# Performance work log

Hardware: AMD Instinct MI355X
Metric: run time of the kernel (lower is better)

The kernel has to match this reference:

```python
import jax, jax.numpy as jnp
import numpy as np

EPS = 1e-9  # Dice BatchNormalization epsilon


def dice(x, alpha):
    # Keras BatchNormalization(axis=-1, center=False, scale=False) in training
    # mode: normalize over all axes except the last using batch statistics.
    mean = jnp.mean(x, axis=(0, 1), keepdims=True)
    var = jnp.var(x, axis=(0, 1), keepdims=True)
    x_normed = (x - mean) * jax.lax.rsqrt(var + EPS)
    p = jax.nn.sigmoid(x_normed)
    return alpha * (1.0 - p) * x + p * x


def setup_inputs() -> dict:
    key = jax.random.key(0)
    ks = jax.random.split(key, 11)
    B, T, D = 512, 2048, 20
    keys_ = jax.random.normal(ks[0], (B, T, D), dtype=jnp.float32)
    query = jax.random.normal(ks[1], (B, 1, D), dtype=jnp.float32)
    mask = jax.random.randint(ks[2], (B, T), 0, 2) > 0
    # DNN tower weights: hidden dims 80 -> 32 -> 16, attention head 16 -> 1
    W0 = jax.random.normal(ks[3], (80, 32), dtype=jnp.float32) * 0.1
    b0 = jax.random.normal(ks[4], (32,), dtype=jnp.float32) * 0.1
    a0 = jax.random.normal(ks[5], (32,), dtype=jnp.float32) * 0.1
    W1 = jax.random.normal(ks[6], (32, 16), dtype=jnp.float32) * 0.1
    b1 = jax.random.normal(ks[7], (16,), dtype=jnp.float32) * 0.1
    a1 = jax.random.normal(ks[8], (16,), dtype=jnp.float32) * 0.1
    wk = jax.random.normal(ks[9], (16, 1), dtype=jnp.float32) * 0.1
    bk = jax.random.normal(ks[10], (1,), dtype=jnp.float32) * 0.1
    return {"keys": keys_, "query": query, "mask": mask,
            "W0": W0, "b0": b0, "a0": a0,
            "W1": W1, "b1": b1, "a1": a1,
            "wk": wk, "bk": bk}


def reference(keys, query, mask, W0, b0, a0, W1, b1, a1, wk, bk):
    B, T, D = keys.shape
    # repeat query along the key/time axis: [B,1,D] -> [B,T,D]
    queries = jnp.broadcast_to(query, (B, T, D))
    # local-activation features: [B,T,4D] = [B,T,80]
    att = jnp.concatenate([queries, keys, queries - keys, queries * keys], axis=-1)
    # DNN tower with Dice activations (dropout is identity at inference)
    h = dice(att @ W0 + b0, a0)   # [B,T,32]
    h = dice(h @ W1 + b1, a1)     # [B,T,16]
    score = h @ wk + bk           # [B,T,1]
    outputs = jnp.transpose(score, (0, 2, 1))  # [B,1,T]
    # NOTE: the original code computes the masked scores into self.outputs but
    # then (weight_normalization=False, return_score=False) overwrites it with
    # matmul(outputs, keys) using the UNMASKED scores -- we reproduce that.
    return jnp.matmul(outputs, keys)  # [B,1,D]
```

## Files before the change

kernel.cpp:

```cpp
#include <hip/hip_runtime.h>


#define BB 512
#define TT 2048
#define DD 20
#define C0 32
#define C1 16

#define NTH 256
#define NPOS 4
#define POSB (NTH * NPOS)
#define NBLK (TT / POSB)

#define WS_SUM0 0
#define WS_SQ0 32
#define WS_SUM1 64
#define WS_SQ1 80
#define WS_SCALE0 96
#define WS_SHIFT0 128
#define WS_SCALE1 160
#define WS_SHIFT1 176
#define WS_BLOB 192
#define BLOB_J 24
#define BLOB_B (C0 * BLOB_J)

#define PIN(x) asm volatile("" : "+v"(x))

__device__ __forceinline__ float fast_sigmoid(float x) {
    return __builtin_amdgcn_rcpf(1.0f + __expf(-x));
}

__device__ __forceinline__ void load_krow(const float* __restrict__ row,
                                          float* kk) {
    const float4* kr = (const float4*)row;
    float4 a = kr[0], b = kr[1], c = kr[2], d = kr[3], e = kr[4];
    kk[0] = a.x; kk[1] = a.y; kk[2] = a.z; kk[3] = a.w;
    kk[4] = b.x; kk[5] = b.y; kk[6] = b.z; kk[7] = b.w;
    kk[8] = c.x; kk[9] = c.y; kk[10] = c.z; kk[11] = c.w;
    kk[12] = d.x; kk[13] = d.y; kk[14] = d.z; kk[15] = d.w;
    kk[16] = e.x; kk[17] = e.y; kk[18] = e.z; kk[19] = e.w;
}

__global__ void prep_kernel(const float* __restrict__ query,
                            const float* __restrict__ W0,
                            const float* __restrict__ b0,
                            float* __restrict__ blob) {
    const int b = blockIdx.x * 2 + (threadIdx.x >> 5);
    const int j = threadIdx.x & 31;
    float cj = b0[j];
    float* dst = blob + (size_t)b * BLOB_B + j * BLOB_J;
#pragma unroll
    for (int d = 0; d < DD; ++d) {
        float w_q = W0[d * C0 + j];
        float w_k = W0[(DD + d) * C0 + j];
        float w_d = W0[(2 * DD + d) * C0 + j];
        float w_p = W0[(3 * DD + d) * C0 + j];
        float qd = query[b * DD + d];
        dst[d] = w_k - w_d + qd * w_p;
        cj = fmaf(qd, w_q + w_d, cj);
    }
    dst[20] = cj;
}

__global__ __launch_bounds__(256, 2) void pass1_kernel(
    const float* __restrict__ keys, const float* __restrict__ blob,
    float* __restrict__ ws) {
    const int b = blockIdx.x >> 2, chunk = blockIdx.x & 3;
    const int tid = threadIdx.x, wave = tid >> 6, lane = tid & 63;
    const int j0 = wave * 8;
    const float* wb = blob + (size_t)b * BLOB_B;
    const float* kbase = keys + ((size_t)b * TT + chunk * (TT / 4)) * DD;

    float wM[8][DD], cj8[8];
#pragma unroll
    for (int jj = 0; jj < 8; ++jj) {
        load_krow(wb + (j0 + jj) * BLOB_J, wM[jj]);
        cj8[jj] = wb[(j0 + jj) * BLOB_J + 20];
    }
#pragma unroll
    for (int jj = 0; jj < 8; ++jj) {
        PIN(cj8[jj]);
#pragma unroll
        for (int d = 0; d < DD; ++d) PIN(wM[jj][d]);
    }

    float s[8], q[8];
#pragma unroll
    for (int v = 0; v < 8; ++v) { s[v] = 0.f; q[v] = 0.f; }

#pragma unroll 1
    for (int it = 0; it < (TT / 4) / 64; ++it) {
        float kk[DD];
        load_krow(kbase + (size_t)(it * 64 + lane) * DD, kk);
#pragma unroll
        for (int jj = 0; jj < 8; ++jj) {
            float h = cj8[jj];
#pragma unroll
            for (int d = 0; d < DD; ++d) h = fmaf(kk[d], wM[jj][d], h);
            s[jj] += h;
            q[jj] = fmaf(h, h, q[jj]);
        }
    }
    float mine = 0.f;
#pragma unroll
    for (int v = 0; v < 16; ++v) {
        float val = (v < 8) ? s[v] : q[v - 8];
#pragma unroll
        for (int o = 32; o >= 1; o >>= 1) val += __shfl_xor(val, o);
        if (lane == v) mine = val;
    }
    __shared__ float red[64];
    if (lane < 16) {
        int j = j0 + (lane & 7);
        red[(lane < 8 ? 0 : 32) + j] = mine;
    }
    __syncthreads();
    if (tid < 64) atomicAdd(&ws[WS_SUM0 + tid], red[tid]);
}

__global__ void finalize_kernel(float* __restrict__ ws, int nch, int sumOff,
                                int sqOff, int scOff, int shOff) {
    int j = threadIdx.x;
    if (j < nch) {
        const float invN = 1.0f / (float)(BB * TT);
        float mean = ws[sumOff + j] * invN;
        float ex2 = ws[sqOff + j] * invN;
        float var = ex2 - mean * mean;
        float sc = rsqrtf(var + 1e-9f);
        ws[scOff + j] = sc;
        ws[shOff + j] = -mean * sc;
    }
}

#define STAGE_WEIGHTS()                                                      \
    for (int idx = tid; idx < C0 * 24; idx += NTH) {                         \
        int j = idx / 24, r = idx - j * 24;                                  \
        float v;                                                             \
        if (r < 21) v = blob[(size_t)b * BLOB_B + j * BLOB_J + r];           \
        else if (r == 21) v = ws[WS_SCALE0 + j];                             \
        else if (r == 22) v = ws[WS_SHIFT0 + j];                             \
        else v = a0[j];                                                      \
        lw[idx] = v;                                                         \
    }                                                                        \
    for (int idx = tid; idx < C0 * C1; idx += NTH) lw1[idx] = W1[idx];

#define LOAD_AND_PIN_KEYS()                                                  \
    const float* kbase = keys + ((size_t)b * TT + chunk * POSB) * DD;        \
    float kk[NPOS][DD];                                                      \
    _Pragma("unroll") for (int pp = 0; pp < NPOS; ++pp)                      \
        load_krow(kbase + (size_t)(tid + pp * NTH) * DD, kk[pp]);            \
    _Pragma("unroll") for (int pp = 0; pp < NPOS; ++pp)                      \
        _Pragma("unroll") for (int d = 0; d < DD; ++d) PIN(kk[pp][d]);

#define TOWER_JLOOP()                                                        \
    _Pragma("unroll 1") for (int j = 0; j < C0; ++j) {                       \
        const float4* wv = (const float4*)&lw[j * 24];                       \
        float4 A = wv[0], B = wv[1], Cc = wv[2], E = wv[3], F = wv[4],       \
               P = wv[5];                                                    \
        const float4* uv = (const float4*)&lw1[j * C1];                      \
        float4 U0 = uv[0], U1 = uv[1], U2 = uv[2], U3 = uv[3];               \
        float wr[DD] = {A.x,  A.y,  A.z,  A.w,  B.x,  B.y,  B.z,             \
                        B.w,  Cc.x, Cc.y, Cc.z, Cc.w, E.x,  E.y,             \
                        E.z,  E.w,  F.x,  F.y,  F.z,  F.w};                  \
        float ur[C1] = {U0.x, U0.y, U0.z, U0.w, U1.x, U1.y, U1.z, U1.w,      \
                        U2.x, U2.y, U2.z, U2.w, U3.x, U3.y, U3.z, U3.w};     \
        float h[NPOS];                                                       \
        _Pragma("unroll") for (int pp = 0; pp < NPOS; ++pp) {                \
            float hh = P.x;                                                  \
            _Pragma("unroll") for (int d = 0; d < DD; ++d)                   \
                hh = fmaf(kk[pp][d], wr[d], hh);                             \
            h[pp] = hh;                                                      \
        }                                                                    \
        _Pragma("unroll") for (int pp = 0; pp < NPOS; ++pp) {                \
            float pr = fast_sigmoid(fmaf(h[pp], P.y, P.z));                  \
            float h0d = h[pp] * (P.w + pr * (1.0f - P.w));                   \
            _Pragma("unroll") for (int c = 0; c < C1; ++c)                   \
                h1[pp][c] = fmaf(h0d, ur[c], h1[pp][c]);                     \
        }                                                                    \
    }

__global__ __launch_bounds__(NTH, 2) void pass2_kernel(
    const float* __restrict__ keys, const float* __restrict__ blob,
    const float* __restrict__ a0, const float* __restrict__ W1,
    const float* __restrict__ b1, float* __restrict__ ws) {
    const int b = blockIdx.x >> 1, chunk = blockIdx.x & 1;
    const int tid = threadIdx.x, wave = tid >> 6, lane = tid & 63;
    __shared__ float lw[C0 * 24];
    __shared__ float lw1[C0 * C1];
    __shared__ float red[4][32];
    STAGE_WEIGHTS()
    __syncthreads();

    LOAD_AND_PIN_KEYS()

    float h1[NPOS][C1];
#pragma unroll
    for (int pp = 0; pp < NPOS; ++pp)
#pragma unroll
        for (int c = 0; c < C1; ++c) h1[pp][c] = 0.f;

    TOWER_JLOOP()

    float s1[C1], q1[C1];
#pragma unroll
    for (int c = 0; c < C1; ++c) {
        float bc = b1[c], sv = 0.f, qv = 0.f;
#pragma unroll
        for (int pp = 0; pp < NPOS; ++pp) {
            float v = h1[pp][c] + bc;
            sv += v;
            qv = fmaf(v, v, qv);
        }
        s1[c] = sv;
        q1[c] = qv;
    }
    float mine = 0.f;
#pragma unroll
    for (int v = 0; v < 32; ++v) {
        float val = (v < C1) ? s1[v] : q1[v - C1];
#pragma unroll
        for (int o = 32; o >= 1; o >>= 1) val += __shfl_xor(val, o);
        if (lane == v) mine = val;
    }
    if (lane < 32) red[wave][lane] = mine;
    __syncthreads();
    if (tid < 32)
        atomicAdd(&ws[WS_SUM1 + tid],
                  red[0][tid] + red[1][tid] + red[2][tid] + red[3][tid]);
}

__global__ __launch_bounds__(NTH, 2) void pass3_kernel(
    const float* __restrict__ keys, const float* __restrict__ blob,
    const float* __restrict__ a0, const float* __restrict__ W1,
    const float* __restrict__ b1, const float* __restrict__ a1,
    const float* __restrict__ wk, const float* __restrict__ bk,
    const float* __restrict__ ws, float* __restrict__ out) {
    const int b = blockIdx.x >> 1, chunk = blockIdx.x & 1;
    const int tid = threadIdx.x, wave = tid >> 6, lane = tid & 63;
    __shared__ float lw[C0 * 24];
    __shared__ float lw1[C0 * C1];
    __shared__ float ld1[C1 * 4];
    __shared__ float red[4][DD];
    STAGE_WEIGHTS()
    if (tid < C1) {
        ld1[tid * 4 + 0] = ws[WS_SCALE1 + tid];
        ld1[tid * 4 + 1] = ws[WS_SHIFT1 + tid];
        ld1[tid * 4 + 2] = a1[tid];
        ld1[tid * 4 + 3] = wk[tid];
    }
    __syncthreads();

    LOAD_AND_PIN_KEYS()

    float h1[NPOS][C1];
#pragma unroll
    for (int pp = 0; pp < NPOS; ++pp)
#pragma unroll
        for (int c = 0; c < C1; ++c) h1[pp][c] = 0.f;

    TOWER_JLOOP()

    const float bkv = bk[0];
    float oacc[DD];
#pragma unroll
    for (int d = 0; d < DD; ++d) oacc[d] = 0.f;
#pragma unroll
    for (int pp = 0; pp < NPOS; ++pp) {
        float score = bkv;
#pragma unroll
        for (int c = 0; c < C1; ++c) {
            float v = h1[pp][c] + b1[c];
            float pr = fast_sigmoid(fmaf(v, ld1[c * 4 + 0], ld1[c * 4 + 1]));
            float al = ld1[c * 4 + 2];
            float hd = v * (al + pr * (1.0f - al));
            score = fmaf(hd, ld1[c * 4 + 3], score);
        }
#pragma unroll
        for (int d = 0; d < DD; ++d) oacc[d] = fmaf(score, kk[pp][d], oacc[d]);
    }
    float mine = 0.f;
#pragma unroll
    for (int v = 0; v < DD; ++v) {
        float val = oacc[v];
#pragma unroll
        for (int o = 32; o >= 1; o >>= 1) val += __shfl_xor(val, o);
        if (lane == v) mine = val;
    }
    if (lane < DD) red[wave][lane] = mine;
    __syncthreads();
    if (tid < DD)
        atomicAdd(&out[b * DD + tid],
                  red[0][tid] + red[1][tid] + red[2][tid] + red[3][tid]);
}

extern "C" void kernel_launch(void* const* d_in, const int* in_sizes, int n_in,
                              void* d_out, int out_size, void* d_ws,
                              size_t ws_size, hipStream_t stream) {
    const float* keys = (const float*)d_in[0];
    const float* query = (const float*)d_in[1];
    const float* W0 = (const float*)d_in[3];
    const float* b0 = (const float*)d_in[4];
    const float* a0 = (const float*)d_in[5];
    const float* W1 = (const float*)d_in[6];
    const float* b1 = (const float*)d_in[7];
    const float* a1 = (const float*)d_in[8];
    const float* wk = (const float*)d_in[9];
    const float* bk = (const float*)d_in[10];
    float* out = (float*)d_out;
    float* ws = (float*)d_ws;
    float* blob = ws + WS_BLOB;

    hipMemsetAsync(ws, 0, 96 * sizeof(float), stream);
    hipMemsetAsync(out, 0, (size_t)out_size * sizeof(float), stream);

    prep_kernel<<<BB / 2, 64, 0, stream>>>(query, W0, b0, blob);

    pass1_kernel<<<BB * 4, 256, 0, stream>>>(keys, blob, ws);
    finalize_kernel<<<1, 32, 0, stream>>>(ws, 32, WS_SUM0, WS_SQ0, WS_SCALE0,
                                          WS_SHIFT0);
    pass2_kernel<<<BB * NBLK, NTH, 0, stream>>>(keys, blob, a0, W1, b1, ws);
    finalize_kernel<<<1, 16, 0, stream>>>(ws, 16, WS_SUM1, WS_SQ1, WS_SCALE1,
                                          WS_SHIFT1);
    pass3_kernel<<<BB * NBLK, NTH, 0, stream>>>(keys, blob, a0, W1, b1, a1, wk,
                                                bk, ws, out);
}
```

Measured before the change: 290.6 us.

## Restructure pass1 per batch, read weights from scalar memory, spread stat atomics

Pass1 now gives one block per batch row. Each thread holds four key rows in registers and loops over all 32 channels, reading the per-batch weights directly from global memory (wave-uniform, so they can go through scalar loads) instead of pinning 160 weights in VGPRs. Passes 2 and 3 drop the shared-memory weight staging and the __syncthreads, and read blob, W1 and stats directly as uniform loads. The statistic atomics are spread over 8 slots to reduce contention, and finalize sums the slots. Pass1 now has fewer blocks (512), which may lower occupancy, and its accumulator register pressure rises.

```diff
diff --git a/kernel.cpp b/kernel.cpp
--- a/kernel.cpp
+++ b/kernel.cpp
@@ -10,17 +10,16 @@
 #define NTH 256
 #define NPOS 4
 #define POSB (NTH * NPOS)
-#define NBLK (TT / POSB)
-
-#define WS_SUM0 0
-#define WS_SQ0 32
-#define WS_SUM1 64
-#define WS_SQ1 80
-#define WS_SCALE0 96
-#define WS_SHIFT0 128
-#define WS_SCALE1 160
-#define WS_SHIFT1 176
-#define WS_BLOB 192
+#define NSLOT 8
+
+#define WS_P1 0
+#define WS_P2 512
+#define WS_SCALE0 768
+#define WS_SHIFT0 800
+#define WS_SCALE1 832
+#define WS_SHIFT1 848
+#define WS_ZERO_N 768
+#define WS_BLOB 896
 #define BLOB_J 24
 #define BLOB_B (C0 * BLOB_J)
 
@@ -62,87 +61,77 @@
     dst[20] = cj;
 }
 
-__global__ __launch_bounds__(256, 2) void pass1_kernel(
+__global__ __launch_bounds__(NTH, 2) void pass1_kernel(
     const float* __restrict__ keys, const float* __restrict__ blob,
-    float* __restrict__ ws) {
-    const int b = blockIdx.x >> 2, chunk = blockIdx.x & 3;
-    const int tid = threadIdx.x, wave = tid >> 6, lane = tid & 63;
-    const int j0 = wave * 8;
-    const float* wb = blob + (size_t)b * BLOB_B;
-    const float* kbase = keys + ((size_t)b * TT + chunk * (TT / 4)) * DD;
-
-    float wM[8][DD], cj8[8];
-#pragma unroll
-    for (int jj = 0; jj < 8; ++jj) {
-        load_krow(wb + (j0 + jj) * BLOB_J, wM[jj]);
-        cj8[jj] = wb[(j0 + jj) * BLOB_J + 20];
-    }
-#pragma unroll
-    for (int jj = 0; jj < 8; ++jj) {
-        PIN(cj8[jj]);
-#pragma unroll
-        for (int d = 0; d < DD; ++d) PIN(wM[jj][d]);
-    }
-
-    float s[8], q[8];
-#pragma unroll
-    for (int v = 0; v < 8; ++v) { s[v] = 0.f; q[v] = 0.f; }
+    float* __restrict__ sums) {
+    const int b = blockIdx.x;
+    const int tid = threadIdx.x, lane = tid & 63;
+    const float* bA = blob + (size_t)b * BLOB_B;
+    const float* kbase = keys + (size_t)b * TT * DD;
+
+    float s[C0], q[C0];
+#pragma unroll
+    for (int j = 0; j < C0; ++j) { s[j] = 0.f; q[j] = 0.f; }
 
 #pragma unroll 1
-    for (int it = 0; it < (TT / 4) / 64; ++it) {
-        float kk[DD];
-        load_krow(kbase + (size_t)(it * 64 + lane) * DD, kk);
-#pragma unroll
-        for (int jj = 0; jj < 8; ++jj) {
-            float h = cj8[jj];
-#pragma unroll
-            for (int d = 0; d < DD; ++d) h = fmaf(kk[d], wM[jj][d], h);
-            s[jj] += h;
-            q[jj] = fmaf(h, h, q[jj]);
-        }
-    }
-    float mine = 0.f;
-#pragma unroll
-    for (int v = 0; v < 16; ++v) {
-        float val = (v < 8) ? s[v] : q[v - 8];
+    for (int r = 0; r < TT / POSB; ++r) {
+        float kk[NPOS][DD];
+#pragma unroll
+        for (int pp = 0; pp < NPOS; ++pp)
+            load_krow(kbase + (size_t)(r * POSB + tid + pp * NTH) * DD,
+                      kk[pp]);
+#pragma unroll
+        for (int pp = 0; pp < NPOS; ++pp)
+#pragma unroll
+            for (int d = 0; d < DD; ++d) PIN(kk[pp][d]);
+#pragma unroll
+        for (int j = 0; j < C0; ++j) {
+            const float* wr = bA + j * BLOB_J;
+            const float cj = wr[20];
+            float sv = 0.f, qv = 0.f;
+#pragma unroll
+            for (int pp = 0; pp < NPOS; ++pp) {
+                float hh = cj;
+#pragma unroll
+                for (int d = 0; d < DD; ++d)
+                    hh = fmaf(kk[pp][d], wr[d], hh);
+                sv += hh;
+                qv = fmaf(hh, hh, qv);
+            }
+            s[j] += sv;
+            q[j] += qv;
+        }
+    }
+    float redv = 0.f;
+#pragma unroll
+    for (int v = 0; v < 2 * C0; ++v) {
+        float val = (v < C0) ? s[v] : q[v - C0];
 #pragma unroll
         for (int o = 32; o >= 1; o >>= 1) val += __shfl_xor(val, o);
-        if (lane == v) mine = val;
-    }
-    __shared__ float red[64];
-    if (lane < 16) {
-        int j = j0 + (lane & 7);
-        red[(lane < 8 ? 0 : 32) + j] = mine;
-    }
-    __syncthreads();
-    if (tid < 64) atomicAdd(&ws[WS_SUM0 + tid], red[tid]);
-}
-
-__global__ void finalize_kernel(float* __restrict__ ws, int nch, int sumOff,
-                                int sqOff, int scOff, int shOff) {
+        if (lane == v) redv = val;
+    }
+    atomicAdd(&sums[WS_P1 + (blockIdx.x & (NSLOT - 1)) * (2 * C0) + lane],
+              redv);
+}
+
+__global__ void finalize_kernel(float* __restrict__ ws, int nch, int srcOff,
+                                int scOff, int shOff) {
     int j = threadIdx.x;
     if (j < nch) {
+        float s = 0.f, q = 0.f;
+#pragma unroll
+        for (int k = 0; k < NSLOT; ++k) {
+            s += ws[srcOff + k * 2 * nch + j];
+            q += ws[srcOff + k * 2 * nch + nch + j];
+        }
         const float invN = 1.0f / (float)(BB * TT);
-        float mean = ws[sumOff + j] * invN;
-        float ex2 = ws[sqOff + j] * invN;
-        float var = ex2 - mean * mean;
-        float sc = rsqrtf(var + 1e-9f);
-        ws[scOff + j] = sc;
-        ws[shOff + j] = -mean * sc;
-    }
-}
-
-#define STAGE_WEIGHTS()                                                      \
-    for (int idx = tid; idx < C0 * 24; idx += NTH) {                         \
-        int j = idx / 24, r = idx - j * 24;                                  \
-        float v;                                                             \
-        if (r < 21) v = blob[(size_t)b * BLOB_B + j * BLOB_J + r];           \
-        else if (r == 21) v = ws[WS_SCALE0 + j];                             \
-        else if (r == 22) v = ws[WS_SHIFT0 + j];                             \
-        else v = a0[j];                                                      \
-        lw[idx] = v;                                                         \
-    }                                                                        \
-    for (int idx = tid; idx < C0 * C1; idx += NTH) lw1[idx] = W1[idx];
+        float mean = s * invN;
+        float var = q * invN - mean * mean;
+        float scv = rsqrtf(var + 1e-9f);
+        ws[scOff + j] = scv;
+        ws[shOff + j] = -mean * scv;
+    }
+}
 
 #define LOAD_AND_PIN_KEYS()                                                  \
     const float* kbase = keys + ((size_t)b * TT + chunk * POSB) * DD;        \
@@ -154,26 +143,23 @@
 
 #define TOWER_JLOOP()                                                        \
     _Pragma("unroll 1") for (int j = 0; j < C0; ++j) {                       \
-        const float4* wv = (const float4*)&lw[j * 24];                       \
-        float4 A = wv[0], B = wv[1], Cc = wv[2], E = wv[3], F = wv[4],       \
-               P = wv[5];                                                    \
-        const float4* uv = (const float4*)&lw1[j * C1];                      \
-        float4 U0 = uv[0], U1 = uv[1], U2 = uv[2], U3 = uv[3];               \
-        float wr[DD] = {A.x,  A.y,  A.z,  A.w,  B.x,  B.y,  B.z,             \
-                        B.w,  Cc.x, Cc.y, Cc.z, Cc.w, E.x,  E.y,             \
-                        E.z,  E.w,  F.x,  F.y,  F.z,  F.w};                  \
-        float ur[C1] = {U0.x, U0.y, U0.z, U0.w, U1.x, U1.y, U1.z, U1.w,      \
-                        U2.x, U2.y, U2.z, U2.w, U3.x, U3.y, U3.z, U3.w};     \
+        const float* wr = bA + j * BLOB_J;                                   \
+        const float* ur = W1 + j * C1;                                       \
+        const float cj = wr[20];                                             \
+        const float sc = stats[WS_SCALE0 + j];                               \
+        const float sh = stats[WS_SHIFT0 + j];                               \
+        const float al = a0[j];                                              \
+        const float nal = 1.0f - al;                                         \
         float h[NPOS];                                                       \
         _Pragma("unroll") for (int pp = 0; pp < NPOS; ++pp) {                \
-            float hh = P.x;                                                  \
+            float hh = cj;                                                   \
             _Pragma("unroll") for (int d = 0; d < DD; ++d)                   \
                 hh = fmaf(kk[pp][d], wr[d], hh);                             \
             h[pp] = hh;                                                      \
         }                                                                    \
         _Pragma("unroll") for (int pp = 0; pp < NPOS; ++pp) {                \
-            float pr = fast_sigmoid(fmaf(h[pp], P.y, P.z));                  \
-            float h0d = h[pp] * (P.w + pr * (1.0f - P.w));                   \
+            float pr = fast_sigmoid(fmaf(h[pp], sc, sh));                    \
+            float h0d = h[pp] * fmaf(pr, nal, al);                           \
             _Pragma("unroll") for (int c = 0; c < C1; ++c)                   \
                 h1[pp][c] = fmaf(h0d, ur[c], h1[pp][c]);                     \
         }                                                                    \
@@ -182,14 +168,11 @@
 __global__ __launch_bounds__(NTH, 2) void pass2_kernel(
     const float* __restrict__ keys, const float* __restrict__ blob,
     const float* __restrict__ a0, const float* __restrict__ W1,
-    const float* __restrict__ b1, float* __restrict__ ws) {
+    const float* __restrict__ b1, const float* __restrict__ stats,
+    float* __restrict__ sums) {
     const int b = blockIdx.x >> 1, chunk = blockIdx.x & 1;
-    const int tid = threadIdx.x, wave = tid >> 6, lane = tid & 63;
-    __shared__ float lw[C0 * 24];
-    __shared__ float lw1[C0 * C1];
-    __shared__ float red[4][32];
-    STAGE_WEIGHTS()
-    __syncthreads();
+    const int tid = threadIdx.x, lane = tid & 63;
+    const float* bA = blob + (size_t)b * BLOB_B;
 
     LOAD_AND_PIN_KEYS()
 
@@ -214,19 +197,17 @@
         s1[c] = sv;
         q1[c] = qv;
     }
-    float mine = 0.f;
-#pragma unroll
-    for (int v = 0; v < 32; ++v) {
+    float redv = 0.f;
+#pragma unroll
+    for (int v = 0; v < 2 * C1; ++v) {
         float val = (v < C1) ? s1[v] : q1[v - C1];
 #pragma unroll
         for (int o = 32; o >= 1; o >>= 1) val += __shfl_xor(val, o);
-        if (lane == v) mine = val;
-    }
-    if (lane < 32) red[wave][lane] = mine;
-    __syncthreads();
-    if (tid < 32)
-        atomicAdd(&ws[WS_SUM1 + tid],
-                  red[0][tid] + red[1][tid] + red[2][tid] + red[3][tid]);
+        if (lane == v) redv = val;
+    }
+    if (lane < 2 * C1)
+        atomicAdd(&sums[WS_P2 + (blockIdx.x & (NSLOT - 1)) * (2 * C1) + lane],
+                  redv);
 }
 
 __global__ __launch_bounds__(NTH, 2) void pass3_kernel(
@@ -234,21 +215,10 @@
     const float* __restrict__ a0, const float* __restrict__ W1,
     const float* __restrict__ b1, const float* __restrict__ a1,
     const float* __restrict__ wk, const float* __restrict__ bk,
-    const float* __restrict__ ws, float* __restrict__ out) {
+    const float* __restrict__ stats, float* __restrict__ out) {
     const int b = blockIdx.x >> 1, chunk = blockIdx.x & 1;
-    const int tid = threadIdx.x, wave = tid >> 6, lane = tid & 63;
-    __shared__ float lw[C0 * 24];
-    __shared__ float lw1[C0 * C1];
-    __shared__ float ld1[C1 * 4];
-    __shared__ float red[4][DD];
-    STAGE_WEIGHTS()
-    if (tid < C1) {
-        ld1[tid * 4 + 0] = ws[WS_SCALE1 + tid];
-        ld1[tid * 4 + 1] = ws[WS_SHIFT1 + tid];
-        ld1[tid * 4 + 2] = a1[tid];
-        ld1[tid * 4 + 3] = wk[tid];
-    }
-    __syncthreads();
+    const int tid = threadIdx.x, lane = tid & 63;
+    const float* bA = blob + (size_t)b * BLOB_B;
 
     LOAD_AND_PIN_KEYS()
 
@@ -270,27 +240,25 @@
 #pragma unroll
         for (int c = 0; c < C1; ++c) {
             float v = h1[pp][c] + b1[c];
-            float pr = fast_sigmoid(fmaf(v, ld1[c * 4 + 0], ld1[c * 4 + 1]));
-            float al = ld1[c * 4 + 2];
-            float hd = v * (al + pr * (1.0f - al));
-            score = fmaf(hd, ld1[c * 4 + 3], score);
-        }
-#pragma unroll
-        for (int d = 0; d < DD; ++d) oacc[d] = fmaf(score, kk[pp][d], oacc[d]);
-    }
-    float mine = 0.f;
+            float pr = fast_sigmoid(
+                fmaf(v, stats[WS_SCALE1 + c], stats[WS_SHIFT1 + c]));
+            float al = a1[c];
+            float hd = v * fmaf(pr, 1.0f - al, al);
+            score = fmaf(hd, wk[c], score);
+        }
+#pragma unroll
+        for (int d = 0; d < DD; ++d)
+            oacc[d] = fmaf(score, kk[pp][d], oacc[d]);
+    }
+    float redv = 0.f;
 #pragma unroll
     for (int v = 0; v < DD; ++v) {
         float val = oacc[v];
 #pragma unroll
         for (int o = 32; o >= 1; o >>= 1) val += __shfl_xor(val, o);
-        if (lane == v) mine = val;
-    }
-    if (lane < DD) red[wave][lane] = mine;
-    __syncthreads();
-    if (tid < DD)
-        atomicAdd(&out[b * DD + tid],
-                  red[0][tid] + red[1][tid] + red[2][tid] + red[3][tid]);
+        if (lane == v) redv = val;
+    }
+    if (lane < DD) atomicAdd(&out[b * DD + lane], redv);
 }
 
 extern "C" void kernel_launch(void* const* d_in, const int* in_sizes, int n_in,
@@ -310,17 +278,15 @@
     float* ws = (float*)d_ws;
     float* blob = ws + WS_BLOB;
 
-    hipMemsetAsync(ws, 0, 96 * sizeof(float), stream);
+    hipMemsetAsync(ws, 0, WS_ZERO_N * sizeof(float), stream);
     hipMemsetAsync(out, 0, (size_t)out_size * sizeof(float), stream);
 
     prep_kernel<<<BB / 2, 64, 0, stream>>>(query, W0, b0, blob);
 
-    pass1_kernel<<<BB * 4, 256, 0, stream>>>(keys, blob, ws);
-    finalize_kernel<<<1, 32, 0, stream>>>(ws, 32, WS_SUM0, WS_SQ0, WS_SCALE0,
-                                          WS_SHIFT0);
-    pass2_kernel<<<BB * NBLK, NTH, 0, stream>>>(keys, blob, a0, W1, b1, ws);
-    finalize_kernel<<<1, 16, 0, stream>>>(ws, 16, WS_SUM1, WS_SQ1, WS_SCALE1,
-                                          WS_SHIFT1);
-    pass3_kernel<<<BB * NBLK, NTH, 0, stream>>>(keys, blob, a0, W1, b1, a1, wk,
-                                                bk, ws, out);
-}
+    pass1_kernel<<<BB, NTH, 0, stream>>>(keys, blob, ws);
+    finalize_kernel<<<1, 32, 0, stream>>>(ws, C0, WS_P1, WS_SCALE0, WS_SHIFT0);
+    pass2_kernel<<<BB * 2, NTH, 0, stream>>>(keys, blob, a0, W1, b1, ws, ws);
+    finalize_kernel<<<1, 16, 0, stream>>>(ws, C1, WS_P2, WS_SCALE1, WS_SHIFT1);
+    pass3_kernel<<<BB * 2, NTH, 0, stream>>>(keys, blob, a0, W1, b1, a1, wk,
+                                             bk, ws, out);
+}
```

Measured after the change: 279.9 us. 3.7% less time.
